# Kernel optimization log

Measured on AMD Instinct MI355X. Metric: run time of the kernel, lower is better.

The kernel has to match this reference:

```python
import jax, jax.numpy as jnp
import numpy as np

N, F, FP, K = 4096, 512, 64, 8
ALPHA = 0.2  # leaky relu slope
NEG_INF = -1e16


def setup_inputs() -> dict:
    key = jax.random.key(0)
    k1, k2, k3, k4 = jax.random.split(key, 4)
    gain = np.sqrt(2.0 / (1.0 + ALPHA ** 2))
    node_matrix = jax.random.normal(k1, (N, F), dtype=jnp.float32)
    adjacency_matrix = jax.random.randint(k2, (N, N), 0, 2, dtype=jnp.int32)
    W = jax.random.normal(k3, (K, F, FP), dtype=jnp.float32) * (gain * np.sqrt(2.0 / (F + FP)))
    a = jax.random.normal(k4, (K, 2 * FP, 1), dtype=jnp.float32) * (gain * np.sqrt(2.0 / (2 * FP + 1)))
    return {"node_matrix": node_matrix, "adjacency_matrix": adjacency_matrix, "W": W, "a": a}


def reference(node_matrix, adjacency_matrix, W, a):
    # hidden_repr: [K, N, F']
    h = jnp.einsum('nf,kfp->knp', node_matrix, W)
    a_src = a[:, :FP, 0]   # applied to attended-to node j (first half -> row vector)
    a_dst = a[:, FP:, 0]   # applied to query node i (second half -> column vector)
    f1 = jnp.einsum('knp,kp->kn', h, a_src)  # [K, N] scores for j
    f2 = jnp.einsum('knp,kp->kn', h, a_dst)  # [K, N] scores for i
    # e[k, i, j] = LeakyReLU(f2[k, i] + f1[k, j])  -> [K, N, N]
    e = jax.nn.leaky_relu(f2[:, :, None] + f1[:, None, :], negative_slope=ALPHA)
    e = jnp.where(adjacency_matrix[None, :, :] > 0, e, NEG_INF)
    att = jax.nn.softmax(e, axis=-1)
    out = jnp.einsum('knm,kmp->knp', att, h)  # [K, N, F']
    # concat heads along feature dim -> [N, K*F']
    return jnp.transpose(out, (1, 0, 2)).reshape(N, K * FP)
```

## Files before the change

kernel.cpp:

```cpp
#include <hip/hip_runtime.h>

#define N 4096
#define F 512
#define FP 64
#define K 8
#define KFP 512
#define LOG2E 1.44269504088896f

typedef __attribute__((ext_vector_type(8))) short short8;
typedef __attribute__((ext_vector_type(4))) float f32x4;
typedef __attribute__((ext_vector_type(2))) float f32x2;

__device__ __forceinline__ unsigned short f2bs(float x) {
  union { __bf16 b; unsigned short u; } u;
  u.b = (__bf16)x;
  return u.u;
}

#if __has_builtin(__builtin_amdgcn_exp2f)
#define EXP2(x) __builtin_amdgcn_exp2f(x)
#else
#define EXP2(x) __expf((x) * 0.6931471805599453f)
#endif

__device__ __forceinline__ f32x2 pk_add(f32x2 a, f32x2 b) {
  f32x2 d;
  asm("v_pk_add_f32 %0, %1, %2" : "=v"(d) : "v"(a), "v"(b));
  return d;
}
__device__ __forceinline__ f32x2 pk_mul(f32x2 a, f32x2 b) {
  f32x2 d;
  asm("v_pk_mul_f32 %0, %1, %2" : "=v"(d) : "v"(a), "v"(b));
  return d;
}

__device__ __forceinline__ float mask_w(float w, unsigned mb, int off) {
  return __int_as_float(__float_as_int(w) & __builtin_amdgcn_sbfe((int)mb, off, 1));
}

#define GLOAD_LDS(src, dst) \
  __builtin_amdgcn_global_load_lds( \
      (const __attribute__((address_space(1))) void*)(src), \
      (__attribute__((address_space(3))) void*)(dst), 16, 0, 0)

__global__ __launch_bounds__(256) void prep_fused(const float* __restrict__ X,
                                                  unsigned short* __restrict__ Xb,
                                                  const float* __restrict__ W,
                                                  unsigned short* __restrict__ Wt) {
  __shared__ unsigned short WT16[64][66];
  const int t = threadIdx.x;
  if (blockIdx.x < 1024) {
    const int idx = (blockIdx.x * 256 + t) * 8;
    const float4 v0 = *reinterpret_cast<const float4*>(&X[idx]);
    const float4 v1 = *reinterpret_cast<const float4*>(&X[idx + 4]);
    unsigned short o[8] = {f2bs(v0.x), f2bs(v0.y), f2bs(v0.z), f2bs(v0.w),
                           f2bs(v1.x), f2bs(v1.y), f2bs(v1.z), f2bs(v1.w)};
    *reinterpret_cast<uint4*>(&Xb[idx]) = *reinterpret_cast<uint4*>(&o[0]);
    return;
  }
  const int bid = blockIdx.x - 1024;
  const int k = bid >> 3;
  const int f0 = (bid & 7) * 64;
#pragma unroll
  for (int j = 0; j < 16; j++) {
    const int idx = j * 256 + t;
    const int fl = idx >> 6, p = idx & 63;
    WT16[p][fl] = f2bs(W[(k * F + f0 + fl) * FP + p]);
  }
  __syncthreads();
  const int p = t >> 2, uc = t & 3;
  unsigned short tmp[16];
#pragma unroll
  for (int j = 0; j < 16; j++) tmp[j] = WT16[p][uc * 16 + j];
  unsigned short* dst = &Wt[(k * 64 + p) * F + f0 + uc * 16];
  *reinterpret_cast<uint4*>(dst)     = *reinterpret_cast<uint4*>(&tmp[0]);
  *reinterpret_cast<uint4*>(dst + 8) = *reinterpret_cast<uint4*>(&tmp[8]);
}

__global__ __launch_bounds__(256, 2) void gemm_h(
    const unsigned short* __restrict__ Xb, const unsigned short* __restrict__ Wt,
    const float* __restrict__ a, unsigned short* __restrict__ h_bT,
    float* __restrict__ f1, float* __restrict__ f2,
    const int* __restrict__ adj, unsigned long long* __restrict__ adjb) {
  __shared__ __align__(16) unsigned char AT[2][8192];
  __shared__ __align__(16) unsigned char BT[2][8192];
  __shared__ float F1L[2][64], F2L[2][64];

  const int t = threadIdx.x;
  const int k = blockIdx.x & 7;
  const int n0 = (blockIdx.x >> 3) * 64;
  const int wave = t >> 6, lane = t & 63;
  const int cg = wave >> 1, ng = wave & 1;
  const int col = lane & 15, kg = lane >> 4;
  const unsigned short* __restrict__ Wk = Wt + (size_t)k * 64 * F;

  f32x4 acc[2][2];
#pragma unroll
  for (int i = 0; i < 2; i++)
#pragma unroll
    for (int j = 0; j < 2; j++) acc[i][j] = (f32x4){0.f, 0.f, 0.f, 0.f};

  auto stage = [&](int tt, int buf) {
    const int f0 = tt * 64;
#pragma unroll
    for (int m = 0; m < 2; m++) {
      const int g = wave * 128 + m * 64 + lane;
      const int row = g >> 3, pu = g & 7;
      const int u = pu ^ (row & 7);
      GLOAD_LDS(Wk + (size_t)row * F + f0 + u * 8,
                AT[buf] + (wave * 128 + m * 64) * 16);
      GLOAD_LDS(Xb + (size_t)(n0 + row) * F + f0 + u * 8,
                BT[buf] + (wave * 128 + m * 64) * 16);
    }
  };

  auto compute = [&](int buf) {
#pragma unroll
    for (int ks = 0; ks < 2; ks++) {
      const int u0 = ks * 4 + kg;
      short8 af[2], bf[2];
#pragma unroll
      for (int i = 0; i < 2; i++) {
        const int rowA = cg * 32 + i * 16 + col;
        af[i] = *reinterpret_cast<const short8*>(
            AT[buf] + (rowA * 8 + (u0 ^ (rowA & 7))) * 16);
        const int rowB = ng * 32 + i * 16 + col;
        bf[i] = *reinterpret_cast<const short8*>(
            BT[buf] + (rowB * 8 + (u0 ^ (rowB & 7))) * 16);
      }
#pragma unroll
      for (int i = 0; i < 2; i++)
#pragma unroll
        for (int j = 0; j < 2; j++)
          acc[i][j] = __builtin_amdgcn_mfma_f32_16x16x32_bf16(af[i], bf[j], acc[i][j], 0, 0, 0);
    }
  };

  int adjv[16];
  const int wb_wave = blockIdx.x * 512 + wave * 128;
  auto adj_load = [&](int c) {
    const int* p = adj + (size_t)(wb_wave + c * 16) * 64 + lane;
#pragma unroll
    for (int x = 0; x < 16; x++) adjv[x] = p[x * 64];
  };
  auto adj_process = [&](int c) {
    unsigned long long ms[16];
#pragma unroll
    for (int x = 0; x < 16; x++) ms[x] = __ballot(adjv[x] > 0);
    if (lane == 0) {
#pragma unroll
      for (int x = 0; x < 16; x++) adjb[wb_wave + c * 16 + x] = ms[x];
    }
  };

  stage(0, 0);
  adj_load(0);
  for (int tt = 0; tt < F / 64; ++tt) {
    const int cur = tt & 1;
    __builtin_amdgcn_s_barrier();
    __builtin_amdgcn_sched_barrier(0);
    if (tt + 1 < F / 64) {
      stage(tt + 1, 1 - cur);
      asm volatile("s_waitcnt vmcnt(4)" ::: "memory");
    } else {
      asm volatile("s_waitcnt vmcnt(0)" ::: "memory");
    }
    __builtin_amdgcn_s_barrier();
    __builtin_amdgcn_sched_barrier(0);
    if (tt >= 1) {
      adj_process(tt - 1);
      adj_load(tt);
    }
    compute(cur);
  }
  asm volatile("s_waitcnt vmcnt(0)" ::: "memory");
  adj_process(7);

  float p1[2] = {0.f, 0.f}, p2[2] = {0.f, 0.f};
#pragma unroll
  for (int i = 0; i < 2; i++) {
#pragma unroll
    for (int r = 0; r < 4; r++) {
      const int p = cg * 32 + i * 16 + kg * 4 + r;
      const float as = a[k * 128 + p];
      const float ad = a[k * 128 + 64 + p];
#pragma unroll
      for (int j = 0; j < 2; j++) {
        const float v = acc[i][j][r];
        h_bT[(size_t)(k * 64 + p) * N + n0 + ng * 32 + j * 16 + col] = f2bs(v);
        p1[j] = fmaf(v, as, p1[j]);
        p2[j] = fmaf(v, ad, p2[j]);
      }
    }
  }
#pragma unroll
  for (int j = 0; j < 2; j++) {
    p1[j] += __shfl_xor(p1[j], 16); p1[j] += __shfl_xor(p1[j], 32);
    p2[j] += __shfl_xor(p2[j], 16); p2[j] += __shfl_xor(p2[j], 32);
    if (kg == 0) {
      F1L[cg][ng * 32 + j * 16 + col] = p1[j];
      F2L[cg][ng * 32 + j * 16 + col] = p2[j];
    }
  }
  __syncthreads();
  if (t < 64) {
    f1[k * N + n0 + t] = (F1L[0][t] + F1L[1][t]) * LOG2E;
    f2[k * N + n0 + t] = (F2L[0][t] + F2L[1][t]) * LOG2E;
  }
}

__global__ __launch_bounds__(256, 4) void attn_mfma(
    const unsigned short* __restrict__ h_bT, const float* __restrict__ f1,
    const float* __restrict__ f2, const unsigned long long* __restrict__ adjb,
    float* __restrict__ out) {
  __shared__ __align__(16) unsigned char SMEM[32768];
  __shared__ float DL[4][32];

  const int tid = threadIdx.x;
  const int k = blockIdx.x & 7;
  const int i0 = (blockIdx.x >> 3) * 32;
  const int jq = tid >> 6, lane = tid & 63;
  const int col = lane & 15, kg = lane >> 4;

  const float* __restrict__ f1k = f1 + k * N;
  const unsigned char* __restrict__ hbb =
      (const unsigned char*)(h_bT + (size_t)k * 64 * N);

  const float f2r0 = f2[k * N + i0 + col];
  const float f2r1 = f2[k * N + i0 + 16 + col];
  const f32x2 f2r0_2 = {f2r0, f2r0};
  const f32x2 f2r1_2 = {f2r1, f2r1};
  const f32x2 c02 = {0.2f, 0.2f};
  const unsigned long long* __restrict__ ar0 = adjb + (size_t)(i0 + col) * 64;
  const unsigned long long* __restrict__ ar1 = adjb + (size_t)(i0 + 16 + col) * 64;

  f32x4 acc[2][4];
  f32x4 accden[2];
#pragma unroll
  for (int a = 0; a < 2; a++) {
    accden[a] = (f32x4){0.f, 0.f, 0.f, 0.f};
#pragma unroll
    for (int n = 0; n < 4; n++) acc[a][n] = (f32x4){0.f, 0.f, 0.f, 0.f};
  }
  short8 bones;
#pragma unroll
  for (int e = 0; e < 8; e++) bones[e] = (short)0x3F80;

  unsigned char* MY = SMEM + jq * 8192;
  const int jqbase = jq * 1024;

  auto stage = [&](int jg) {
#pragma unroll
    for (int m = 0; m < 8; m++) {
      const int row = m * 8 + (lane >> 3);
      const int phys = lane & 7;
      const int u = phys ^ (row & 7);
      GLOAD_LDS(hbb + (size_t)row * (N * 2) + (jqbase + jg * 64 + u * 8) * 2,
                MY + m * 1024);
    }
  };

  stage(0);
  for (int jg = 0; jg < 16; ++jg) {
    const uint2 aw0 = *reinterpret_cast<const uint2*>(ar0 + jq * 16 + jg);
    const uint2 aw1 = *reinterpret_cast<const uint2*>(ar1 + jq * 16 + jg);

    short8 Af0[2], Af1[2];
#pragma unroll
    for (int ks = 0; ks < 2; ks++) {
      const int jb = jqbase + jg * 64 + ks * 32 + kg * 8;
      const float4 fa = *reinterpret_cast<const float4*>(&f1k[jb]);
      const float4 fb = *reinterpret_cast<const float4*>(&f1k[jb + 4]);
      const unsigned m0 = ks ? aw0.y : aw0.x;
      const unsigned m1 = ks ? aw1.y : aw1.x;
      const f32x2 prs[4] = {{fa.x, fa.y}, {fa.z, fa.w}, {fb.x, fb.y}, {fb.z, fb.w}};
      union { unsigned u[4]; short8 s; } A0, A1;
#pragma unroll
      for (int e2 = 0; e2 < 4; e2++) {
        const f32x2 t0 = pk_add(prs[e2], f2r0_2);
        const f32x2 t1 = pk_add(prs[e2], f2r1_2);
        const f32x2 u0 = pk_mul(t0, c02);
        const f32x2 u1 = pk_mul(t1, c02);
        float w0a = EXP2(fmaxf(t0.x, u0.x));
        float w0b = EXP2(fmaxf(t0.y, u0.y));
        float w1a = EXP2(fmaxf(t1.x, u1.x));
        float w1b = EXP2(fmaxf(t1.y, u1.y));
        const int ob = kg * 8 + 2 * e2;
        w0a = mask_w(w0a, m0, ob);     w0b = mask_w(w0b, m0, ob + 1);
        w1a = mask_w(w1a, m1, ob);     w1b = mask_w(w1b, m1, ob + 1);
        asm("v_cvt_pk_bf16_f32 %0, %1, %2" : "=v"(A0.u[e2]) : "v"(w0a), "v"(w0b));
        asm("v_cvt_pk_bf16_f32 %0, %1, %2" : "=v"(A1.u[e2]) : "v"(w1a), "v"(w1b));
      }
      Af0[ks] = A0.s;
      Af1[ks] = A1.s;
    }

    asm volatile("s_waitcnt vmcnt(0)" ::: "memory");
    __builtin_amdgcn_sched_barrier(0);
    short8 bfr[2][4];
#pragma unroll
    for (int ks = 0; ks < 2; ks++)
#pragma unroll
      for (int n = 0; n < 4; n++) {
        const int row_b = n * 16 + col;
        const int u = ks * 4 + kg;
        bfr[ks][n] = *reinterpret_cast<const short8*>(
            MY + row_b * 128 + (u ^ (row_b & 7)) * 16);
      }
    asm volatile("s_waitcnt lgkmcnt(0)" ::: "memory");
    __builtin_amdgcn_sched_barrier(0);
    if (jg + 1 < 16) stage(jg + 1);

    __builtin_amdgcn_s_setprio(1);
#pragma unroll
    for (int ks = 0; ks < 2; ks++) {
      accden[0] = __builtin_amdgcn_mfma_f32_16x16x32_bf16(Af0[ks], bones, accden[0], 0, 0, 0);
      accden[1] = __builtin_amdgcn_mfma_f32_16x16x32_bf16(Af1[ks], bones, accden[1], 0, 0, 0);
#pragma unroll
      for (int n = 0; n < 4; n++) {
        acc[0][n] = __builtin_amdgcn_mfma_f32_16x16x32_bf16(Af0[ks], bfr[ks][n], acc[0][n], 0, 0, 0);
        acc[1][n] = __builtin_amdgcn_mfma_f32_16x16x32_bf16(Af1[ks], bfr[ks][n], acc[1][n], 0, 0, 0);
      }
    }
    __builtin_amdgcn_s_setprio(0);
  }

  __syncthreads();

  float* CL = (float*)SMEM;
  if (col == 0) {
#pragma unroll
    for (int a = 0; a < 2; a++)
#pragma unroll
      for (int r = 0; r < 4; r++) DL[jq][a * 16 + kg * 4 + r] = accden[a][r];
  }
  if (jq != 0) {
#pragma unroll
    for (int a = 0; a < 2; a++)
#pragma unroll
      for (int n = 0; n < 4; n++)
#pragma unroll
        for (int r = 0; r < 4; r++)
          CL[((jq - 1) * 32 + a * 16 + kg * 4 + r) * 66 + n * 16 + col] = acc[a][n][r];
  }
  __syncthreads();
  if (jq == 0) {
#pragma unroll
    for (int a = 0; a < 2; a++) {
#pragma unroll
      for (int r = 0; r < 4; r++) {
        const int il = a * 16 + kg * 4 + r;
        const float den = DL[0][il] + DL[1][il] + DL[2][il] + DL[3][il];
        const float rinv = 1.f / den;
#pragma unroll
        for (int n = 0; n < 4; n++) {
          float v = acc[a][n][r];
          v += CL[(0 * 32 + il) * 66 + n * 16 + col];
          v += CL[(1 * 32 + il) * 66 + n * 16 + col];
          v += CL[(2 * 32 + il) * 66 + n * 16 + col];
          out[(size_t)(i0 + il) * KFP + k * 64 + n * 16 + col] = v * rinv;
        }
      }
    }
  }
}

extern "C" void kernel_launch(void* const* d_in, const int* in_sizes, int n_in,
                              void* d_out, int out_size, void* d_ws, size_t ws_size,
                              hipStream_t stream) {
  const float* X   = (const float*)d_in[0];
  const int*   adj = (const int*)d_in[1];
  const float* W   = (const float*)d_in[2];
  const float* a   = (const float*)d_in[3];
  float* out = (float*)d_out;

  char* ws = (char*)d_ws;
  unsigned short* h_bT = (unsigned short*)(ws);
  float* f1  = (float*)(ws + 4194304);
  float* f2  = (float*)(ws + 4325376);
  unsigned long long* adjb = (unsigned long long*)(ws + 4456448);
  unsigned short* Wt = (unsigned short*)(ws + 6553600);
  unsigned short* Xb = (unsigned short*)d_out;

  hipLaunchKernelGGL(prep_fused, dim3(1024 + K * (F / 64)), dim3(256), 0, stream,
                     X, Xb, W, Wt);
  hipLaunchKernelGGL(gemm_h, dim3(K * (N / 64)), dim3(256), 0, stream,
                     Xb, Wt, a, h_bT, f1, f2, adj, adjb);
  hipLaunchKernelGGL(attn_mfma, dim3((N / 32) * K), dim3(256), 0, stream,
                     h_bT, f1, f2, adjb, out);
}
```

Baseline: 83.02 us.

## Double attention row tile per block and prefetch f1/adjacency one step ahead

Each attention block now handles 64 query rows instead of 32, so every staged h tile in LDS feeds twice as many MFMAs and the h traffic per output drops by half. The f1 scores and adjacency bitmask words for the next column group are loaded together with the LDS stage instead of at the start of each iteration, hiding that latency. The epilogue reduction is split into two halves so the larger accumulator set fits in the existing LDS buffer. The cost is roughly twice the accumulator registers, occupancy lowered to 2 blocks per SIMD, and half as many blocks in the grid.

```diff
diff --git a/kernel.cpp b/kernel.cpp
--- a/kernel.cpp
+++ b/kernel.cpp
@@ -17,11 +17,11 @@
   return u.u;
 }
 
-#if __has_builtin(__builtin_amdgcn_exp2f)
-#define EXP2(x) __builtin_amdgcn_exp2f(x)
-#else
-#define EXP2(x) __expf((x) * 0.6931471805599453f)
-#endif
+__device__ __forceinline__ float exp2_asm(float x) {
+  float d;
+  asm("v_exp_f32 %0, %1" : "=v"(d) : "v"(x));
+  return d;
+}
 
 __device__ __forceinline__ f32x2 pk_add(f32x2 a, f32x2 b) {
   f32x2 d;
@@ -209,16 +209,16 @@
   }
 }
 
-__global__ __launch_bounds__(256, 4) void attn_mfma(
+__global__ __launch_bounds__(256, 2) void attn_mfma(
     const unsigned short* __restrict__ h_bT, const float* __restrict__ f1,
     const float* __restrict__ f2, const unsigned long long* __restrict__ adjb,
     float* __restrict__ out) {
   __shared__ __align__(16) unsigned char SMEM[32768];
-  __shared__ float DL[4][32];
+  __shared__ float DL[4][64];
 
   const int tid = threadIdx.x;
   const int k = blockIdx.x & 7;
-  const int i0 = (blockIdx.x >> 3) * 32;
+  const int i0 = (blockIdx.x >> 3) * 64;
   const int jq = tid >> 6, lane = tid & 63;
   const int col = lane & 15, kg = lane >> 4;
 
@@ -226,21 +226,21 @@
   const unsigned char* __restrict__ hbb =
       (const unsigned char*)(h_bT + (size_t)k * 64 * N);
 
-  const float f2r0 = f2[k * N + i0 + col];
-  const float f2r1 = f2[k * N + i0 + 16 + col];
-  const f32x2 f2r0_2 = {f2r0, f2r0};
-  const f32x2 f2r1_2 = {f2r1, f2r1};
+  f32x2 f2r2[4];
+#pragma unroll
+  for (int rg = 0; rg < 4; rg++) {
+    const float v = f2[k * N + i0 + rg * 16 + col];
+    f2r2[rg] = (f32x2){v, v};
+  }
   const f32x2 c02 = {0.2f, 0.2f};
-  const unsigned long long* __restrict__ ar0 = adjb + (size_t)(i0 + col) * 64;
-  const unsigned long long* __restrict__ ar1 = adjb + (size_t)(i0 + 16 + col) * 64;
-
-  f32x4 acc[2][4];
-  f32x4 accden[2];
-#pragma unroll
-  for (int a = 0; a < 2; a++) {
-    accden[a] = (f32x4){0.f, 0.f, 0.f, 0.f};
-#pragma unroll
-    for (int n = 0; n < 4; n++) acc[a][n] = (f32x4){0.f, 0.f, 0.f, 0.f};
+
+  f32x4 acc[4][4];
+  f32x4 accden[4];
+#pragma unroll
+  for (int rg = 0; rg < 4; rg++) {
+    accden[rg] = (f32x4){0.f, 0.f, 0.f, 0.f};
+#pragma unroll
+    for (int n = 0; n < 4; n++) acc[rg][n] = (f32x4){0.f, 0.f, 0.f, 0.f};
   }
   short8 bones;
 #pragma unroll
@@ -260,43 +260,53 @@
     }
   };
 
+  float4 pf[4];
+  uint2 pw[4];
+  auto pload = [&](int jg) {
+    const int jb = jqbase + jg * 64 + kg * 8;
+    pf[0] = *reinterpret_cast<const float4*>(&f1k[jb]);
+    pf[1] = *reinterpret_cast<const float4*>(&f1k[jb + 4]);
+    pf[2] = *reinterpret_cast<const float4*>(&f1k[jb + 32]);
+    pf[3] = *reinterpret_cast<const float4*>(&f1k[jb + 36]);
+#pragma unroll
+    for (int rg = 0; rg < 4; rg++)
+      pw[rg] = *reinterpret_cast<const uint2*>(
+          adjb + (size_t)(i0 + rg * 16 + col) * 64 + jq * 16 + jg);
+  };
+
   stage(0);
+  pload(0);
+#pragma unroll 1
   for (int jg = 0; jg < 16; ++jg) {
-    const uint2 aw0 = *reinterpret_cast<const uint2*>(ar0 + jq * 16 + jg);
-    const uint2 aw1 = *reinterpret_cast<const uint2*>(ar1 + jq * 16 + jg);
-
-    short8 Af0[2], Af1[2];
-#pragma unroll
-    for (int ks = 0; ks < 2; ks++) {
-      const int jb = jqbase + jg * 64 + ks * 32 + kg * 8;
-      const float4 fa = *reinterpret_cast<const float4*>(&f1k[jb]);
-      const float4 fb = *reinterpret_cast<const float4*>(&f1k[jb + 4]);
-      const unsigned m0 = ks ? aw0.y : aw0.x;
-      const unsigned m1 = ks ? aw1.y : aw1.x;
-      const f32x2 prs[4] = {{fa.x, fa.y}, {fa.z, fa.w}, {fb.x, fb.y}, {fb.z, fb.w}};
-      union { unsigned u[4]; short8 s; } A0, A1;
-#pragma unroll
-      for (int e2 = 0; e2 < 4; e2++) {
-        const f32x2 t0 = pk_add(prs[e2], f2r0_2);
-        const f32x2 t1 = pk_add(prs[e2], f2r1_2);
-        const f32x2 u0 = pk_mul(t0, c02);
-        const f32x2 u1 = pk_mul(t1, c02);
-        float w0a = EXP2(fmaxf(t0.x, u0.x));
-        float w0b = EXP2(fmaxf(t0.y, u0.y));
-        float w1a = EXP2(fmaxf(t1.x, u1.x));
-        float w1b = EXP2(fmaxf(t1.y, u1.y));
-        const int ob = kg * 8 + 2 * e2;
-        w0a = mask_w(w0a, m0, ob);     w0b = mask_w(w0b, m0, ob + 1);
-        w1a = mask_w(w1a, m1, ob);     w1b = mask_w(w1b, m1, ob + 1);
-        asm("v_cvt_pk_bf16_f32 %0, %1, %2" : "=v"(A0.u[e2]) : "v"(w0a), "v"(w0b));
-        asm("v_cvt_pk_bf16_f32 %0, %1, %2" : "=v"(A1.u[e2]) : "v"(w1a), "v"(w1b));
-      }
-      Af0[ks] = A0.s;
-      Af1[ks] = A1.s;
-    }
-
     asm volatile("s_waitcnt vmcnt(0)" ::: "memory");
     __builtin_amdgcn_sched_barrier(0);
+
+    short8 Af[2][4];
+#pragma unroll
+    for (int ks = 0; ks < 2; ks++) {
+      const f32x2 prs[4] = {{pf[ks * 2].x, pf[ks * 2].y},
+                            {pf[ks * 2].z, pf[ks * 2].w},
+                            {pf[ks * 2 + 1].x, pf[ks * 2 + 1].y},
+                            {pf[ks * 2 + 1].z, pf[ks * 2 + 1].w}};
+#pragma unroll
+      for (int rg = 0; rg < 4; rg++) {
+        const unsigned m = ks ? pw[rg].y : pw[rg].x;
+        union { unsigned u[4]; short8 s; } A;
+#pragma unroll
+        for (int e2 = 0; e2 < 4; e2++) {
+          const f32x2 t = pk_add(prs[e2], f2r2[rg]);
+          const f32x2 u = pk_mul(t, c02);
+          float wa = exp2_asm(fmaxf(t.x, u.x));
+          float wb = exp2_asm(fmaxf(t.y, u.y));
+          const int ob = kg * 8 + 2 * e2;
+          wa = mask_w(wa, m, ob);
+          wb = mask_w(wb, m, ob + 1);
+          asm("v_cvt_pk_bf16_f32 %0, %1, %2" : "=v"(A.u[e2]) : "v"(wa), "v"(wb));
+        }
+        Af[ks][rg] = A.s;
+      }
+    }
+
     short8 bfr[2][4];
 #pragma unroll
     for (int ks = 0; ks < 2; ks++)
@@ -309,59 +319,76 @@
       }
     asm volatile("s_waitcnt lgkmcnt(0)" ::: "memory");
     __builtin_amdgcn_sched_barrier(0);
-    if (jg + 1 < 16) stage(jg + 1);
+
+    if (jg + 1 < 16) {
+      stage(jg + 1);
+      pload(jg + 1);
+    }
 
     __builtin_amdgcn_s_setprio(1);
 #pragma unroll
-    for (int ks = 0; ks < 2; ks++) {
-      accden[0] = __builtin_amdgcn_mfma_f32_16x16x32_bf16(Af0[ks], bones, accden[0], 0, 0, 0);
-      accden[1] = __builtin_amdgcn_mfma_f32_16x16x32_bf16(Af1[ks], bones, accden[1], 0, 0, 0);
-#pragma unroll
-      for (int n = 0; n < 4; n++) {
-        acc[0][n] = __builtin_amdgcn_mfma_f32_16x16x32_bf16(Af0[ks], bfr[ks][n], acc[0][n], 0, 0, 0);
-        acc[1][n] = __builtin_amdgcn_mfma_f32_16x16x32_bf16(Af1[ks], bfr[ks][n], acc[1][n], 0, 0, 0);
-      }
-    }
+    for (int ks = 0; ks < 2; ks++)
+#pragma unroll
+      for (int rg = 0; rg < 4; rg++) {
+        accden[rg] = __builtin_amdgcn_mfma_f32_16x16x32_bf16(Af[ks][rg], bones, accden[rg], 0, 0, 0);
+#pragma unroll
+        for (int n = 0; n < 4; n++)
+          acc[rg][n] = __builtin_amdgcn_mfma_f32_16x16x32_bf16(Af[ks][rg], bfr[ks][n], acc[rg][n], 0, 0, 0);
+      }
     __builtin_amdgcn_s_setprio(0);
   }
 
   __syncthreads();
 
+  if (col == 0) {
+#pragma unroll
+    for (int rg = 0; rg < 4; rg++)
+#pragma unroll
+      for (int r = 0; r < 4; r++) DL[jq][rg * 16 + kg * 4 + r] = accden[rg][r];
+  }
+
   float* CL = (float*)SMEM;
-  if (col == 0) {
-#pragma unroll
-    for (int a = 0; a < 2; a++)
-#pragma unroll
-      for (int r = 0; r < 4; r++) DL[jq][a * 16 + kg * 4 + r] = accden[a][r];
-  }
-  if (jq != 0) {
-#pragma unroll
-    for (int a = 0; a < 2; a++)
-#pragma unroll
-      for (int n = 0; n < 4; n++)
-#pragma unroll
-        for (int r = 0; r < 4; r++)
-          CL[((jq - 1) * 32 + a * 16 + kg * 4 + r) * 66 + n * 16 + col] = acc[a][n][r];
-  }
-  __syncthreads();
-  if (jq == 0) {
-#pragma unroll
-    for (int a = 0; a < 2; a++) {
-#pragma unroll
-      for (int r = 0; r < 4; r++) {
-        const int il = a * 16 + kg * 4 + r;
-        const float den = DL[0][il] + DL[1][il] + DL[2][il] + DL[3][il];
-        const float rinv = 1.f / den;
-#pragma unroll
-        for (int n = 0; n < 4; n++) {
-          float v = acc[a][n][r];
-          v += CL[(0 * 32 + il) * 66 + n * 16 + col];
-          v += CL[(1 * 32 + il) * 66 + n * 16 + col];
-          v += CL[(2 * 32 + il) * 66 + n * 16 + col];
-          out[(size_t)(i0 + il) * KFP + k * 64 + n * 16 + col] = v * rinv;
+  float rinv[4][4];
+#pragma unroll
+  for (int h = 0; h < 2; ++h) {
+    if (jq != 0) {
+#pragma unroll
+      for (int rg = 0; rg < 4; rg++)
+#pragma unroll
+        for (int nn = 0; nn < 2; nn++)
+#pragma unroll
+          for (int r = 0; r < 4; r++)
+            CL[((jq - 1) * 64 + rg * 16 + kg * 4 + r) * 33 + nn * 16 + col] =
+                acc[rg][h * 2 + nn][r];
+    }
+    __syncthreads();
+    if (jq == 0) {
+      if (h == 0) {
+#pragma unroll
+        for (int rg = 0; rg < 4; rg++)
+#pragma unroll
+          for (int r = 0; r < 4; r++) {
+            const int il = rg * 16 + kg * 4 + r;
+            rinv[rg][r] = 1.f / (DL[0][il] + DL[1][il] + DL[2][il] + DL[3][il]);
+          }
+      }
+#pragma unroll
+      for (int rg = 0; rg < 4; rg++)
+#pragma unroll
+        for (int r = 0; r < 4; r++) {
+          const int il = rg * 16 + kg * 4 + r;
+#pragma unroll
+          for (int nn = 0; nn < 2; nn++) {
+            const int n = h * 2 + nn;
+            float v = acc[rg][n][r];
+            v += CL[(0 * 64 + il) * 33 + nn * 16 + col];
+            v += CL[(1 * 64 + il) * 33 + nn * 16 + col];
+            v += CL[(2 * 64 + il) * 33 + nn * 16 + col];
+            out[(size_t)(i0 + il) * KFP + k * 64 + n * 16 + col] = v * rinv[rg][r];
+          }
         }
-      }
-    }
+    }
+    __syncthreads();
   }
 }
 
@@ -386,6 +413,6 @@
                      X, Xb, W, Wt);
   hipLaunchKernelGGL(gemm_h, dim3(K * (N / 64)), dim3(256), 0, stream,
                      Xb, Wt, a, h_bT, f1, f2, adj, adjb);
-  hipLaunchKernelGGL(attn_mfma, dim3((N / 32) * K), dim3(256), 0, stream,
+  hipLaunchKernelGGL(attn_mfma, dim3((N / 64) * K), dim3(256), 0, stream,
                      h_bT, f1, f2, adjb, out);
 }
```

New measurement: 79.43 us. 1.05x faster.
